# Optimization experiments

Hardware: AMD Instinct MI355X
Metric: run time of the kernel (lower is better)

The kernel has to match this reference:

```python
import jax, jax.numpy as jnp
import numpy as np

HEADS = 8
HDIM = 64
MAX_PEMB = 512


def setup_inputs() -> dict:
    key = jax.random.key(0)
    ks = jax.random.split(key, 6)
    B, S, D = 4, 1024, 512
    return {
        "x": jax.random.normal(ks[0], (B, S, D), jnp.float32),
        "attn_mask": jnp.ones((B, S), jnp.bool_),
        "Wq": jax.random.normal(ks[1], (D, HEADS * HDIM), jnp.float32) * 0.02,
        "Wkv": jax.random.normal(ks[2], (D, 2 * HEADS * HDIM), jnp.float32) * 0.02,
        "Wout": jax.random.normal(ks[3], (HEADS * HDIM, D), jnp.float32) * 0.02,
        "bout": jnp.zeros((D,), jnp.float32),
        "pemb": jax.random.normal(ks[4], (2 * MAX_PEMB + 1, HDIM), jnp.float32) * 0.02,
    }


def reference(x, attn_mask, Wq, Wkv, Wout, bout, pemb):
    # attn_mask is unpacked but unused in the original call(); faithful to source.
    B, S, D = x.shape
    scale = HDIM ** (-0.5)

    q = (x @ Wq).reshape(B, S, HEADS, HDIM).transpose(0, 2, 1, 3)  # [B,H,S,hd]
    kv = x @ Wkv
    k, v = jnp.split(kv, 2, axis=-1)
    k = k.reshape(B, S, HEADS, HDIM).transpose(0, 2, 1, 3)
    v = v.reshape(B, S, HEADS, HDIM).transpose(0, 2, 1, 3)

    attn_score = jnp.einsum('bhqd,bhkd->bhqk', q, k) * scale

    seq = jnp.arange(S)
    dist = jnp.clip(seq[:, None] - seq[None, :], -MAX_PEMB, MAX_PEMB) + MAX_PEMB  # [S,S]
    rel_pemb = pemb[dist]  # [S,S,hd]
    pos_attn = jnp.einsum('bhsd,std->bhst', q, rel_pemb) * scale  # [B,H,S,S]

    attn_probs = jax.nn.softmax(attn_score + pos_attn, axis=-1)
    ctx = jnp.einsum('bhqk,bhkd->bqhd', attn_probs, v).reshape(B, S, HEADS * HDIM)
    return ctx @ Wout + bout
```

## Files before the change

### kernel.cpp

```cpp
#include <hip/hip_runtime.h>
#include <hip/hip_bf16.h>

constexpr int BATCH = 4;
constexpr int SEQ   = 1024;
constexpr int DM    = 512;
constexpr int NH    = 8;
constexpr int HD    = 64;
constexpr int NQKV  = 1536;

typedef unsigned short u16;
typedef __attribute__((ext_vector_type(8))) __bf16 bf8;
typedef __attribute__((ext_vector_type(4))) __bf16 bf4;
typedef __attribute__((ext_vector_type(4))) float  f4;

#define MFMA16(a, b, c) __builtin_amdgcn_mfma_f32_16x16x32_bf16(a, b, c, 0, 0, 0)

#define QSC 0.18033688f

static __device__ __forceinline__ u16 f2b(float f) {
    union { float f; unsigned u; } v; v.f = f;
    unsigned r = v.u + 0x7FFFu + ((v.u >> 16) & 1u);
    return (u16)(r >> 16);
}
static __device__ __forceinline__ float fexp2(float x) {
    return __builtin_amdgcn_exp2f(x);
}
static __device__ __forceinline__ void gl_lds16(const void* g, void* l) {
    __builtin_amdgcn_global_load_lds(
        (const __attribute__((address_space(1))) void*)g,
        (__attribute__((address_space(3))) void*)l, 16, 0, 0);
}

__device__ __forceinline__ void tcvt_tile(const float* __restrict__ in,
                                          u16* __restrict__ out,
                                          int R, int C, int bx, int by, int tid,
                                          float (*t)[33]) {
    int r0 = by * 32, c0 = bx * 32;
    int lc = tid & 31, lr = tid >> 5;
    #pragma unroll
    for (int p = 0; p < 4; p++) {
        int r = lr + p * 8;
        t[r][lc] = in[(size_t)(r0 + r) * C + c0 + lc];
    }
    __syncthreads();
    #pragma unroll
    for (int p = 0; p < 4; p++) {
        int r = lr + p * 8;
        out[(size_t)(c0 + r) * R + r0 + lc] = f2b(t[lc][r]);
    }
}

__global__ __launch_bounds__(256)
void prep(const float* __restrict__ x, const float* __restrict__ Wq,
          const float* __restrict__ Wkv, const float* __restrict__ Wout,
          const float* __restrict__ pemb,
          u16* __restrict__ xb, u16* __restrict__ qkvw,
          u16* __restrict__ Woutt, u16* __restrict__ pembb) {
    __shared__ float t[32][33];
    const int blk = blockIdx.x, tid = threadIdx.x;
    if (blk < 2048) {
        int i = (blk * 256 + tid) * 4;
        float4 v = *(const float4*)(x + i);
        ushort4 o = {f2b(v.x), f2b(v.y), f2b(v.z), f2b(v.w)};
        *(ushort4*)(xb + i) = o;
    } else if (blk < 2113) {
        int i = ((blk - 2048) * 256 + tid) * 4;
        if (i < 1025 * HD) {
            float4 v = *(const float4*)(pemb + i);
            ushort4 o = {f2b(v.x), f2b(v.y), f2b(v.z), f2b(v.w)};
            *(ushort4*)(pembb + i) = o;
        }
    } else if (blk < 2369) {
        int l = blk - 2113;
        tcvt_tile(Wq, qkvw, 512, 512, l & 15, l >> 4, tid, t);
    } else if (blk < 2881) {
        int l = blk - 2369;
        tcvt_tile(Wkv, qkvw + 512 * 512, 512, 1024, l & 31, l >> 5, tid, t);
    } else {
        int l = blk - 2881;
        tcvt_tile(Wout, Woutt, 512, 512, l & 15, l >> 4, tid, t);
    }
}

__global__ __launch_bounds__(256)
void gemm_bt(const u16* __restrict__ A, const u16* __restrict__ Bt,
             int M, int N, int K,
             float* __restrict__ Cf, const float* __restrict__ bias,
             __bf16* __restrict__ qtb, __bf16* __restrict__ ktb,
             __bf16* __restrict__ vtb) {
    __shared__ __align__(16) u16 As[2][64][32];
    __shared__ __align__(16) u16 Bs[2][128][32];
    const int tid = threadIdx.x, w = tid >> 6, lane = tid & 63;
    const int l15 = lane & 15, l4 = lane >> 4;
    const int wr = (w >> 1) * 32, wc = (w & 1) * 64;
    const int bm = blockIdx.y * 64, bn = blockIdx.x * 128;

    f4 acc[2][4];
    #pragma unroll
    for (int i = 0; i < 2; i++)
        #pragma unroll
        for (int j = 0; j < 4; j++) acc[i][j] = (f4){0.f, 0.f, 0.f, 0.f};

    const int rS = lane >> 2;
    const int cS = (lane & 3) * 8;

    for (int k0 = 0; k0 < K; k0 += 64) {
        #pragma unroll
        for (int ks = 0; ks < 2; ks++) {
            gl_lds16(A + (size_t)(bm + w * 16 + rS) * K + k0 + ks * 32 + cS,
                     &As[ks][w * 16][0]);
            gl_lds16(Bt + (size_t)(bn + w * 32 + rS) * K + k0 + ks * 32 + cS,
                     &Bs[ks][w * 32][0]);
            gl_lds16(Bt + (size_t)(bn + w * 32 + 16 + rS) * K + k0 + ks * 32 + cS,
                     &Bs[ks][w * 32 + 16][0]);
        }
        __syncthreads();
        #pragma unroll
        for (int ks = 0; ks < 2; ks++) {
            bf8 af[2], bf[4];
            #pragma unroll
            for (int i = 0; i < 2; i++)
                af[i] = *(const bf8*)&As[ks][wr + i * 16 + l15][l4 * 8];
            #pragma unroll
            for (int j = 0; j < 4; j++)
                bf[j] = *(const bf8*)&Bs[ks][wc + j * 16 + l15][l4 * 8];
            #pragma unroll
            for (int i = 0; i < 2; i++)
                #pragma unroll
                for (int j = 0; j < 4; j++)
                    acc[i][j] = MFMA16(af[i], bf[j], acc[i][j]);
        }
        __syncthreads();
    }
    #pragma unroll
    for (int i = 0; i < 2; i++)
        #pragma unroll
        for (int j = 0; j < 4; j++) {
            const int col = bn + wc + j * 16 + l15;
            const int row0 = bm + wr + i * 16 + l4 * 4;
            if (Cf) {
                #pragma unroll
                for (int reg = 0; reg < 4; reg++)
                    Cf[(size_t)(row0 + reg) * N + col] = acc[i][j][reg] + bias[col];
            } else if (col < 512) {
                int h = col >> 6, d = col & 63;
                #pragma unroll
                for (int reg = 0; reg < 4; reg++) {
                    int row = row0 + reg;
                    int b = row >> 10, t = row & 1023;
                    qtb[((((size_t)(b * 8 + h)) << 10 | t) << 6) | d] =
                        (__bf16)(acc[i][j][reg] * QSC);
                }
            } else if (col < 1024) {
                int h = (col >> 6) - 8, d = col & 63;
                #pragma unroll
                for (int reg = 0; reg < 4; reg++) {
                    int row = row0 + reg;
                    int b = row >> 10, t = row & 1023;
                    ktb[((((size_t)(b * 8 + h)) << 10 | t) << 6) | d] =
                        (__bf16)acc[i][j][reg];
                }
            } else {
                int h = (col >> 6) - 16, d = col & 63;
                int b = row0 >> 10, t = row0 & 1023;
                __bf16 pk[4];
                #pragma unroll
                for (int reg = 0; reg < 4; reg++) pk[reg] = (__bf16)acc[i][j][reg];
                *(ushort4*)&vtb[(((size_t)(b * 8 + h) * 64 + d) << 10) | t] =
                    *(ushort4*)pk;
            }
        }
}

__global__ __launch_bounds__(256)
void attn_mfma(const u16* __restrict__ qtb, const u16* __restrict__ ktb,
               const u16* __restrict__ vtb, const u16* __restrict__ pembb,
               __bf16* __restrict__ ctxb) {
    __shared__ __align__(16) __bf16 Kb[2][64][72];
    __shared__ __align__(16) __bf16 Vb[2][64][72];
    __shared__ __align__(16) __bf16 Ps[64][72];
    __shared__ __align__(16) __bf16 Qd[128][72];

    const int tid = threadIdx.x, w = tid >> 6, lane = tid & 63;
    const int l15 = lane & 15, l4 = lane >> 4;
    const int bh = blockIdx.x, b = bh >> 3;
    const int s0 = blockIdx.y * 64;

    const int xw = l4 << 4;
    const int xr = (l15 >> 2) << 4;

    const int sl0 = w * 16 + l4 * 4;

    const u16* qp = qtb + ((size_t)bh * SEQ + s0 + w * 16 + l15) * HD + l4 * 8;
    bf8 qa0 = *(const bf8*)qp;
    bf8 qa1 = *(const bf8*)(qp + 32);

    #pragma unroll
    for (int pass = 0; pass < 2; pass++) {
        const int jlo = s0 + 449 + pass * 64;
        #pragma unroll
        for (int jt = 0; jt < 4; jt++) {
            int jc = min(1024, max(0, jlo + jt * 16 + l15));
            const u16* pp = pembb + (size_t)jc * HD + l4 * 8;
            bf8 b0 = *(const bf8*)pp;
            bf8 b1 = *(const bf8*)(pp + 32);
            f4 f = (f4){0.f, 0.f, 0.f, 0.f};
            f = MFMA16(qa0, b0, f);
            f = MFMA16(qa1, b1, f);
            int j = jlo + jt * 16 + l15;
            bf4 pk;
            #pragma unroll
            for (int reg = 0; reg < 4; reg++) pk[reg] = (__bf16)f[reg];
            *(bf4*)&Qd[j & 127][sl0] = pk;
        }
    }
    asm volatile("" ::: "memory");

    float l_r[4] = {0.f, 0.f, 0.f, 0.f};
    f4 o[4];
    #pragma unroll
    for (int dt = 0; dt < 4; dt++) o[dt] = (f4){0.f, 0.f, 0.f, 0.f};

    const u16* kbase = ktb + (size_t)bh * SEQ * HD;
    const u16* vbase = vtb + (size_t)bh * HD * SEQ;
    const u16* pbase = pembb + l4 * 8;

    const int sr = tid >> 3, sc = (tid & 7) * 8;

    *(bf8*)&Kb[0][sr][sc]      = *(const bf8*)(kbase + (size_t)sr * HD + sc);
    *(bf8*)&Kb[0][sr + 32][sc] = *(const bf8*)(kbase + (size_t)(sr + 32) * HD + sc);
    *(bf8*)&Vb[0][sr][sc]      = *(const bf8*)(vbase + (size_t)sr * SEQ + sc);
    *(bf8*)&Vb[0][sr + 32][sc] = *(const bf8*)(vbase + (size_t)(sr + 32) * SEQ + sc);
    __syncthreads();

    for (int i = 0; i < 16; i++) {
        const int cur = i & 1, nxt = cur ^ 1;
        const int t0 = i * 64, t1 = t0 + 64;
        const bool pre = (i < 15);
        bf8 kr0, kr1, vr0, vr1, pb0[4], pb1[4];
        const int jlo_next = s0 + 449 - 64 * (i + 1);
        if (pre) {
            kr0 = *(const bf8*)(kbase + (size_t)(t1 + sr) * HD + sc);
            kr1 = *(const bf8*)(kbase + (size_t)(t1 + sr + 32) * HD + sc);
            vr0 = *(const bf8*)(vbase + (size_t)sr * SEQ + t1 + sc);
            vr1 = *(const bf8*)(vbase + (size_t)(sr + 32) * SEQ + t1 + sc);
            #pragma unroll
            for (int jt = 0; jt < 4; jt++) {
                int jc = min(1024, max(0, jlo_next + jt * 16 + l15));
                const u16* pp = pbase + (size_t)jc * HD;
                pb0[jt] = *(const bf8*)pp;
                pb1[jt] = *(const bf8*)(pp + 32);
            }
        }

        f4 s[4];
        #pragma unroll
        for (int jt = 0; jt < 4; jt++) {
            bf8 b0 = *(const bf8*)&Kb[cur][jt * 16 + l15][l4 * 8];
            bf8 b1 = *(const bf8*)&Kb[cur][jt * 16 + l15][32 + l4 * 8];
            f4 acc = (f4){0.f, 0.f, 0.f, 0.f};
            acc = MFMA16(qa0, b0, acc);
            acc = MFMA16(qa1, b1, acc);
            s[jt] = acc;
        }
        bf8 vf0[4], vf1[4];
        #pragma unroll
        for (int dt = 0; dt < 4; dt++) {
            vf0[dt] = *(const bf8*)&Vb[cur][dt * 16 + l15][l4 * 8];
            vf1[dt] = *(const bf8*)&Vb[cur][dt * 16 + l15][32 + l4 * 8];
        }
        const int jbase = s0 - t0 + 512;
        float sc4[4][4];
        #pragma unroll
        for (int jt = 0; jt < 4; jt++) {
            int tl = jt * 16 + l15;
            #pragma unroll
            for (int reg = 0; reg < 4; reg++) {
                int sl = sl0 + reg;
                int j = jbase + sl - tl;
                float p = fexp2(s[jt][reg] + (float)Qd[j & 127][sl]);
                sc4[jt][reg] = p;
                l_r[reg] += p;
            }
        }
        #pragma unroll
        for (int jt = 0; jt < 4; jt++)
            #pragma unroll
            for (int reg = 0; reg < 4; reg++)
                Ps[sl0 + reg][(jt * 16 + l15) ^ xw] = (__bf16)sc4[jt][reg];
        asm volatile("" ::: "memory");
        bf8 pa0 = *(const bf8*)&Ps[w * 16 + l15][(l4 * 8) ^ xr];
        bf8 pa1 = *(const bf8*)&Ps[w * 16 + l15][(32 + l4 * 8) ^ xr];
        #pragma unroll
        for (int dt = 0; dt < 4; dt++) {
            o[dt] = MFMA16(pa0, vf0[dt], o[dt]);
            o[dt] = MFMA16(pa1, vf1[dt], o[dt]);
        }
        if (pre) {
            #pragma unroll
            for (int jt = 0; jt < 4; jt++) {
                f4 f = (f4){0.f, 0.f, 0.f, 0.f};
                f = MFMA16(qa0, pb0[jt], f);
                f = MFMA16(qa1, pb1[jt], f);
                int j = jlo_next + jt * 16 + l15;
                bf4 pk;
                #pragma unroll
                for (int reg = 0; reg < 4; reg++) pk[reg] = (__bf16)f[reg];
                *(bf4*)&Qd[j & 127][sl0] = pk;
            }
            *(bf8*)&Kb[nxt][sr][sc]      = kr0;
            *(bf8*)&Kb[nxt][sr + 32][sc] = kr1;
            *(bf8*)&Vb[nxt][sr][sc]      = vr0;
            *(bf8*)&Vb[nxt][sr + 32][sc] = vr1;
        }
        __syncthreads();
    }
    #pragma unroll
    for (int reg = 0; reg < 4; reg++) {
        float r2 = l_r[reg];
        #pragma unroll
        for (int off = 8; off; off >>= 1) r2 += __shfl_xor(r2, off);
        l_r[reg] = 1.f / r2;
    }
    const int h = bh & 7;
    #pragma unroll
    for (int dt = 0; dt < 4; dt++)
        #pragma unroll
        for (int reg = 0; reg < 4; reg++) {
            int srow = s0 + w * 16 + l4 * 4 + reg;
            float v = o[dt][reg] * l_r[reg];
            ctxb[(size_t)(b * SEQ + srow) * DM + h * HD + dt * 16 + l15] = (__bf16)v;
        }
}

extern "C" void kernel_launch(void* const* d_in, const int* in_sizes, int n_in,
                              void* d_out, int out_size, void* d_ws, size_t ws_size,
                              hipStream_t stream) {
    const float* x    = (const float*)d_in[0];
    const float* Wq   = (const float*)d_in[2];
    const float* Wkv  = (const float*)d_in[3];
    const float* Wout = (const float*)d_in[4];
    const float* bout = (const float*)d_in[5];
    const float* pemb = (const float*)d_in[6];
    float* out = (float*)d_out;

    const int M = BATCH * SEQ;
    u16* p = (u16*)d_ws;
    u16* xb    = p; p += (size_t)M * DM;
    u16* qkvw  = p; p += (size_t)NQKV * DM;
    u16* Woutt = p; p += (size_t)DM * DM;
    u16* pembb = p; p += (size_t)1025 * HD;
    u16* qtb   = p; p += (size_t)M * DM;
    u16* ktb   = p; p += (size_t)M * DM;
    u16* vtb   = p; p += (size_t)M * DM;
    u16* ctxb  = p; p += (size_t)M * DM;

    prep<<<3137, 256, 0, stream>>>(x, Wq, Wkv, Wout, pemb, xb, qkvw, Woutt, pembb);

    gemm_bt<<<dim3(NQKV / 128, M / 64), 256, 0, stream>>>(
        xb, qkvw, M, NQKV, DM, nullptr, nullptr,
        (__bf16*)qtb, (__bf16*)ktb, (__bf16*)vtb);

    attn_mfma<<<dim3(BATCH * NH, SEQ / 64), 256, 0, stream>>>(
        qtb, ktb, vtb, pembb, (__bf16*)ctxb);

    gemm_bt<<<dim3(DM / 128, M / 64), 256, 0, stream>>>(
        ctxb, Woutt, M, DM, DM, out, bout, nullptr, nullptr, nullptr);
}
```

Before: 137.2 us.

## Switch attention kernel to 32x32 MFMA with register-resident P via permlane swap

```diff
diff --git a/kernel.cpp b/kernel.cpp
--- a/kernel.cpp
+++ b/kernel.cpp
@@ -12,8 +12,10 @@
 typedef __attribute__((ext_vector_type(8))) __bf16 bf8;
 typedef __attribute__((ext_vector_type(4))) __bf16 bf4;
 typedef __attribute__((ext_vector_type(4))) float  f4;
+typedef __attribute__((ext_vector_type(16))) float f16v;
 
 #define MFMA16(a, b, c) __builtin_amdgcn_mfma_f32_16x16x32_bf16(a, b, c, 0, 0, 0)
+#define MFMA32(a, b, c) __builtin_amdgcn_mfma_f32_32x32x16_bf16(a, b, c, 0, 0, 0)
 
 #define QSC 0.18033688f
 
@@ -29,6 +31,14 @@
     __builtin_amdgcn_global_load_lds(
         (const __attribute__((address_space(1))) void*)g,
         (__attribute__((address_space(3))) void*)l, 16, 0, 0);
+}
+static __device__ __forceinline__ unsigned cvtpk_bf16(float lo, float hi) {
+    unsigned r;
+    asm("v_cvt_pk_bf16_f32 %0, %1, %2" : "=v"(r) : "v"(lo), "v"(hi));
+    return r;
+}
+static __device__ __forceinline__ void swap32(unsigned &a, unsigned &b) {
+    asm("v_permlane32_swap_b32 %0, %1" : "+v"(a), "+v"(b));
 }
 
 __device__ __forceinline__ void tcvt_tile(const float* __restrict__ in,
@@ -178,53 +188,52 @@
                __bf16* __restrict__ ctxb) {
     __shared__ __align__(16) __bf16 Kb[2][64][72];
     __shared__ __align__(16) __bf16 Vb[2][64][72];
-    __shared__ __align__(16) __bf16 Ps[64][72];
-    __shared__ __align__(16) __bf16 Qd[128][72];
+    __shared__ __align__(16) __bf16 Qd[256][72];
 
     const int tid = threadIdx.x, w = tid >> 6, lane = tid & 63;
-    const int l15 = lane & 15, l4 = lane >> 4;
+    const int l31 = lane & 31, hi = lane >> 5;
+    const int wq = w >> 1, wt = w & 1;
     const int bh = blockIdx.x, b = bh >> 3;
     const int s0 = blockIdx.y * 64;
 
-    const int xw = l4 << 4;
-    const int xr = (l15 >> 2) << 4;
-
-    const int sl0 = w * 16 + l4 * 4;
-
-    const u16* qp = qtb + ((size_t)bh * SEQ + s0 + w * 16 + l15) * HD + l4 * 8;
-    bf8 qa0 = *(const bf8*)qp;
-    bf8 qa1 = *(const bf8*)(qp + 32);
+    bf8 qb[4];
+    {
+        const u16* qp = qtb + ((size_t)bh * SEQ + s0 + wq * 32 + l31) * HD + hi * 8;
+        #pragma unroll
+        for (int st = 0; st < 4; st++) qb[st] = *(const bf8*)(qp + st * 16);
+    }
 
     #pragma unroll
     for (int pass = 0; pass < 2; pass++) {
-        const int jlo = s0 + 449 + pass * 64;
-        #pragma unroll
-        for (int jt = 0; jt < 4; jt++) {
-            int jc = min(1024, max(0, jlo + jt * 16 + l15));
-            const u16* pp = pembb + (size_t)jc * HD + l4 * 8;
-            bf8 b0 = *(const bf8*)pp;
-            bf8 b1 = *(const bf8*)(pp + 32);
-            f4 f = (f4){0.f, 0.f, 0.f, 0.f};
-            f = MFMA16(qa0, b0, f);
-            f = MFMA16(qa1, b1, f);
-            int j = jlo + jt * 16 + l15;
+        const int jr = s0 + 449 + pass * 64 + wt * 32 + l31;
+        const int jc = min(1024, max(0, jr));
+        const u16* pp = pembb + (size_t)jc * HD + hi * 8;
+        f16v acc;
+        #pragma unroll
+        for (int r = 0; r < 16; r++) acc[r] = 0.f;
+        #pragma unroll
+        for (int st = 0; st < 4; st++) {
+            bf8 pj = *(const bf8*)(pp + st * 16);
+            acc = MFMA32(qb[st], pj, acc);
+        }
+        #pragma unroll
+        for (int o4 = 0; o4 < 4; o4++) {
             bf4 pk;
             #pragma unroll
-            for (int reg = 0; reg < 4; reg++) pk[reg] = (__bf16)f[reg];
-            *(bf4*)&Qd[j & 127][sl0] = pk;
-        }
-    }
-    asm volatile("" ::: "memory");
-
-    float l_r[4] = {0.f, 0.f, 0.f, 0.f};
-    f4 o[4];
-    #pragma unroll
-    for (int dt = 0; dt < 4; dt++) o[dt] = (f4){0.f, 0.f, 0.f, 0.f};
+            for (int r = 0; r < 4; r++) pk[r] = (__bf16)acc[o4 * 4 + r];
+            *(bf4*)&Qd[jr & 255][wq * 32 + o4 * 8 + hi * 4] = pk;
+        }
+    }
+
+    float l_lane = 0.f;
+    f16v oo[2];
+    #pragma unroll
+    for (int dt = 0; dt < 2; dt++)
+        #pragma unroll
+        for (int r = 0; r < 16; r++) oo[dt][r] = 0.f;
 
     const u16* kbase = ktb + (size_t)bh * SEQ * HD;
     const u16* vbase = vtb + (size_t)bh * HD * SEQ;
-    const u16* pbase = pembb + l4 * 8;
-
     const int sr = tid >> 3, sc = (tid & 7) * 8;
 
     *(bf8*)&Kb[0][sr][sc]      = *(const bf8*)(kbase + (size_t)sr * HD + sc);
@@ -237,76 +246,73 @@
         const int cur = i & 1, nxt = cur ^ 1;
         const int t0 = i * 64, t1 = t0 + 64;
         const bool pre = (i < 15);
-        bf8 kr0, kr1, vr0, vr1, pb0[4], pb1[4];
-        const int jlo_next = s0 + 449 - 64 * (i + 1);
+        bf8 kr0, kr1, vr0, vr1, pj0, pj1, pj2, pj3;
+        const int jrn = s0 + 449 - 64 * (i + 1) + wt * 32 + l31;
         if (pre) {
             kr0 = *(const bf8*)(kbase + (size_t)(t1 + sr) * HD + sc);
             kr1 = *(const bf8*)(kbase + (size_t)(t1 + sr + 32) * HD + sc);
             vr0 = *(const bf8*)(vbase + (size_t)sr * SEQ + t1 + sc);
             vr1 = *(const bf8*)(vbase + (size_t)(sr + 32) * SEQ + t1 + sc);
-            #pragma unroll
-            for (int jt = 0; jt < 4; jt++) {
-                int jc = min(1024, max(0, jlo_next + jt * 16 + l15));
-                const u16* pp = pbase + (size_t)jc * HD;
-                pb0[jt] = *(const bf8*)pp;
-                pb1[jt] = *(const bf8*)(pp + 32);
-            }
-        }
-
-        f4 s[4];
-        #pragma unroll
-        for (int jt = 0; jt < 4; jt++) {
-            bf8 b0 = *(const bf8*)&Kb[cur][jt * 16 + l15][l4 * 8];
-            bf8 b1 = *(const bf8*)&Kb[cur][jt * 16 + l15][32 + l4 * 8];
-            f4 acc = (f4){0.f, 0.f, 0.f, 0.f};
-            acc = MFMA16(qa0, b0, acc);
-            acc = MFMA16(qa1, b1, acc);
-            s[jt] = acc;
-        }
-        bf8 vf0[4], vf1[4];
-        #pragma unroll
-        for (int dt = 0; dt < 4; dt++) {
-            vf0[dt] = *(const bf8*)&Vb[cur][dt * 16 + l15][l4 * 8];
-            vf1[dt] = *(const bf8*)&Vb[cur][dt * 16 + l15][32 + l4 * 8];
-        }
-        const int jbase = s0 - t0 + 512;
-        float sc4[4][4];
-        #pragma unroll
-        for (int jt = 0; jt < 4; jt++) {
-            int tl = jt * 16 + l15;
-            #pragma unroll
-            for (int reg = 0; reg < 4; reg++) {
-                int sl = sl0 + reg;
-                int j = jbase + sl - tl;
-                float p = fexp2(s[jt][reg] + (float)Qd[j & 127][sl]);
-                sc4[jt][reg] = p;
-                l_r[reg] += p;
-            }
-        }
-        #pragma unroll
-        for (int jt = 0; jt < 4; jt++)
-            #pragma unroll
-            for (int reg = 0; reg < 4; reg++)
-                Ps[sl0 + reg][(jt * 16 + l15) ^ xw] = (__bf16)sc4[jt][reg];
-        asm volatile("" ::: "memory");
-        bf8 pa0 = *(const bf8*)&Ps[w * 16 + l15][(l4 * 8) ^ xr];
-        bf8 pa1 = *(const bf8*)&Ps[w * 16 + l15][(32 + l4 * 8) ^ xr];
-        #pragma unroll
-        for (int dt = 0; dt < 4; dt++) {
-            o[dt] = MFMA16(pa0, vf0[dt], o[dt]);
-            o[dt] = MFMA16(pa1, vf1[dt], o[dt]);
-        }
+            const int jc = min(1024, max(0, jrn));
+            const u16* pp = pembb + (size_t)jc * HD + hi * 8;
+            pj0 = *(const bf8*)(pp);
+            pj1 = *(const bf8*)(pp + 16);
+            pj2 = *(const bf8*)(pp + 32);
+            pj3 = *(const bf8*)(pp + 48);
+        }
+
+        f16v s16;
+        #pragma unroll
+        for (int r = 0; r < 16; r++) s16[r] = 0.f;
+        #pragma unroll
+        for (int st = 0; st < 4; st++) {
+            bf8 ka = *(const bf8*)&Kb[cur][wt * 32 + l31][st * 16 + hi * 8];
+            s16 = MFMA32(ka, qb[st], s16);
+        }
+        bf8 vf00 = *(const bf8*)&Vb[cur][l31][wt * 32 + hi * 8];
+        bf8 vf01 = *(const bf8*)&Vb[cur][l31][wt * 32 + 16 + hi * 8];
+        bf8 vf10 = *(const bf8*)&Vb[cur][32 + l31][wt * 32 + hi * 8];
+        bf8 vf11 = *(const bf8*)&Vb[cur][32 + l31][wt * 32 + 16 + hi * 8];
+
+        const int jcst = (s0 - t0 + 512) + wq * 32 + l31 - wt * 32 - 4 * hi;
+        const __bf16* qdc = &Qd[0][wq * 32 + l31];
+        float p[16];
+        #pragma unroll
+        for (int r = 0; r < 16; r++) {
+            const int pat = (r & 3) + 8 * (r >> 2);
+            const int j = (jcst - pat) & 255;
+            float pv = fexp2(s16[r] + (float)qdc[j * 72]);
+            p[r] = pv;
+            l_lane += pv;
+        }
+        unsigned w00 = cvtpk_bf16(p[0],  p[1]),  w01 = cvtpk_bf16(p[2],  p[3]);
+        unsigned w10 = cvtpk_bf16(p[4],  p[5]),  w11 = cvtpk_bf16(p[6],  p[7]);
+        unsigned w20 = cvtpk_bf16(p[8],  p[9]),  w21 = cvtpk_bf16(p[10], p[11]);
+        unsigned w30 = cvtpk_bf16(p[12], p[13]), w31 = cvtpk_bf16(p[14], p[15]);
+        swap32(w00, w10); swap32(w01, w11);
+        swap32(w20, w30); swap32(w21, w31);
+        union { unsigned u[4]; bf8 v; } pa0, pa1;
+        pa0.u[0] = w00; pa0.u[1] = w01; pa0.u[2] = w10; pa0.u[3] = w11;
+        pa1.u[0] = w20; pa1.u[1] = w21; pa1.u[2] = w30; pa1.u[3] = w31;
+        oo[0] = MFMA32(pa0.v, vf00, oo[0]);
+        oo[0] = MFMA32(pa1.v, vf01, oo[0]);
+        oo[1] = MFMA32(pa0.v, vf10, oo[1]);
+        oo[1] = MFMA32(pa1.v, vf11, oo[1]);
+
         if (pre) {
-            #pragma unroll
-            for (int jt = 0; jt < 4; jt++) {
-                f4 f = (f4){0.f, 0.f, 0.f, 0.f};
-                f = MFMA16(qa0, pb0[jt], f);
-                f = MFMA16(qa1, pb1[jt], f);
-                int j = jlo_next + jt * 16 + l15;
+            f16v rf;
+            #pragma unroll
+            for (int r = 0; r < 16; r++) rf[r] = 0.f;
+            rf = MFMA32(qb[0], pj0, rf);
+            rf = MFMA32(qb[1], pj1, rf);
+            rf = MFMA32(qb[2], pj2, rf);
+            rf = MFMA32(qb[3], pj3, rf);
+            #pragma unroll
+            for (int o4 = 0; o4 < 4; o4++) {
                 bf4 pk;
                 #pragma unroll
-                for (int reg = 0; reg < 4; reg++) pk[reg] = (__bf16)f[reg];
-                *(bf4*)&Qd[j & 127][sl0] = pk;
+                for (int r = 0; r < 4; r++) pk[r] = (__bf16)rf[o4 * 4 + r];
+                *(bf4*)&Qd[jrn & 255][wq * 32 + o4 * 8 + hi * 4] = pk;
             }
             *(bf8*)&Kb[nxt][sr][sc]      = kr0;
             *(bf8*)&Kb[nxt][sr + 32][sc] = kr1;
@@ -315,22 +321,35 @@
         }
         __syncthreads();
     }
-    #pragma unroll
-    for (int reg = 0; reg < 4; reg++) {
-        float r2 = l_r[reg];
-        #pragma unroll
-        for (int off = 8; off; off >>= 1) r2 += __shfl_xor(r2, off);
-        l_r[reg] = 1.f / r2;
-    }
-    const int h = bh & 7;
-    #pragma unroll
-    for (int dt = 0; dt < 4; dt++)
-        #pragma unroll
-        for (int reg = 0; reg < 4; reg++) {
-            int srow = s0 + w * 16 + l4 * 4 + reg;
-            float v = o[dt][reg] * l_r[reg];
-            ctxb[(size_t)(b * SEQ + srow) * DM + h * HD + dt * 16 + l15] = (__bf16)v;
-        }
+
+    float lsum = l_lane + __shfl_xor(l_lane, 32);
+    float* Os = (float*)&Qd[0][0];
+    float* Ls = Os + 4096;
+    if (lane < 32) Ls[(wq * 2 + wt) * 32 + l31] = lsum;
+    if (wt == 0) {
+        #pragma unroll
+        for (int dt = 0; dt < 2; dt++)
+            #pragma unroll
+            for (int r = 0; r < 16; r++) {
+                const int q = (r & 3) + 8 * (r >> 2) + 4 * hi;
+                Os[(wq * 32 + q) * 64 + dt * 32 + l31] = oo[dt][r];
+            }
+    }
+    __syncthreads();
+    if (wt == 1) {
+        const int h = bh & 7;
+        #pragma unroll
+        for (int r = 0; r < 16; r++) {
+            const int q = (r & 3) + 8 * (r >> 2) + 4 * hi;
+            const float li = 1.f / (Ls[wq * 64 + q] + Ls[wq * 64 + 32 + q]);
+            #pragma unroll
+            for (int dt = 0; dt < 2; dt++) {
+                float v = (oo[dt][r] + Os[(wq * 32 + q) * 64 + dt * 32 + l31]) * li;
+                ctxb[(size_t)(b * SEQ + s0 + wq * 32 + q) * DM + h * HD + dt * 32 + l31]
+                    = (__bf16)v;
+            }
+        }
+    }
 }
 
 extern "C" void kernel_launch(void* const* d_in, const int* in_sizes, int n_in,
```

Result: faster. 127.3 us (-7.2%).
